# Performance work log

Hardware: AMD Instinct MI355X
Metric: run time of the kernel (lower is better)

## Reference

```python
import jax, jax.numpy as jnp
import numpy as np

B, C, H, W = 4, 256, 64, 64
DQK = C // 4


def setup_inputs() -> dict:
    key = jax.random.key(0)
    ks = jax.random.split(key, 5)
    s = 0.05
    x = jax.random.normal(ks[0], (B, C, H, W), dtype=jnp.float32)
    Wq = jax.random.normal(ks[1], (DQK, C), dtype=jnp.float32) * s
    Wk = jax.random.normal(ks[2], (DQK, C), dtype=jnp.float32) * s
    Wv = jax.random.normal(ks[3], (C, C), dtype=jnp.float32) * s
    bq = jnp.zeros((DQK,), jnp.float32)
    bk = jnp.zeros((DQK,), jnp.float32)
    bv = jnp.zeros((C,), jnp.float32)
    gamma = jnp.zeros((1,), jnp.float32)
    return {"x": x, "Wq": Wq, "bq": bq, "Wk": Wk, "bk": bk,
            "Wv": Wv, "bv": bv, "gamma": gamma}


def reference(x, Wq, bq, Wk, bk, Wv, bv, gamma):
    b, c, h, w = x.shape
    n = h * w
    xf = x.reshape(b, c, n)                      # [B, C, N]
    # 1x1 convs == per-pixel linear projections
    q = jnp.einsum('dc,bcn->bnd', Wq, xf) + bq   # [B, N, Dqk]
    k = jnp.einsum('dc,bcn->bdn', Wk, xf) + bk[None, :, None]  # [B, Dqk, N]
    v = jnp.einsum('ec,bcn->ben', Wv, xf) + bv[None, :, None]  # [B, C, N]
    energy = jnp.einsum('bnd,bdm->bnm', q, k)    # [B, N, N]
    attn = jax.nn.softmax(energy, axis=-1)       # softmax over keys
    # out[b,c,i] = sum_j v[b,c,j] * attn[b,i,j]
    out = jnp.einsum('bcj,bij->bci', v, attn)    # [B, C, N]
    out = out.reshape(b, c, h, w)
    return gamma * out + x
```

## Files before the change

kernel.cpp:

```cpp
#include <hip/hip_runtime.h>

#define B_ 4
#define C_ 256
#define N_ 4096
#define D_ 64

typedef __bf16 bf16x8 __attribute__((ext_vector_type(8)));
typedef float floatx4 __attribute__((ext_vector_type(4)));
typedef unsigned short ushort8v __attribute__((ext_vector_type(8)));
typedef unsigned short ushort4v __attribute__((ext_vector_type(4)));
typedef unsigned short ushort2v __attribute__((ext_vector_type(2)));

static __device__ __forceinline__ unsigned short f2bf(float f) {
    unsigned int u = __builtin_bit_cast(unsigned int, f);
    u += 0x7fffu + ((u >> 16) & 1u);
    return (unsigned short)(u >> 16);
}
static __device__ __forceinline__ float bf2f(unsigned short h) {
    unsigned int u = ((unsigned int)h) << 16;
    return __builtin_bit_cast(float, u);
}

#define GLOAD16(gp, lp)                                                      \
    __builtin_amdgcn_global_load_lds(                                        \
        (const __attribute__((address_space(1))) void*)(gp),                 \
        (__attribute__((address_space(3))) void*)(lp), 16, 0, 0)

__global__ __launch_bounds__(256) void convert_w(
    const float* __restrict__ Wq, const float* __restrict__ Wk,
    const float* __restrict__ Wv, unsigned short* __restrict__ WbfA)
{
    int tid = blockIdx.x * 256 + threadIdx.x;
    int p0  = tid * 4;
    int j0   = p0 & 7;
    int lane = (p0 >> 3) & 63;
    int sidx = p0 >> 9;
    int ft = sidx >> 3, ks = sidx & 7;
    int m  = lane & 15, g = lane >> 4;
    int f  = 16*ft + m;
    int c  = 32*ks + 8*g + j0;
    const float* src = (f < 64)  ? (Wq + (size_t)f * C_)
                     : (f < 128) ? (Wk + (size_t)(f - 64) * C_)
                                 : (Wv + (size_t)(f - 128) * C_);
    float4 v = *(const float4*)(src + c);
    ushort4v u;
    u[0] = f2bf(v.x); u[1] = f2bf(v.y); u[2] = f2bf(v.z); u[3] = f2bf(v.w);
    *(ushort4v*)(WbfA + p0) = u;
}

__global__ __launch_bounds__(256, 3) void proj_kernel(
    const float* __restrict__ x, const unsigned short* __restrict__ WbfA,
    const float* __restrict__ bq, const float* __restrict__ bk,
    const float* __restrict__ bv,
    unsigned short* __restrict__ Qg, unsigned short* __restrict__ Kg,
    unsigned short* __restrict__ Vg)
{
    __shared__ __align__(16) unsigned short smem[64 * 264];
    unsigned short* xs = smem;
    unsigned short* Lt = smem;

    const int n0 = blockIdx.x * 64;
    const int f0 = blockIdx.y * 128;
    const int b  = blockIdx.z;
    const int t  = threadIdx.x;
    const int w  = t >> 6;
    const int lane = t & 63;
    const int g  = lane >> 4;
    const int m  = lane & 15;

#pragma unroll
    for (int k = 0; k < 8; ++k) {
        int e  = t + 256 * k;
        int cp = e >> 4;
        int c  = 2 * cp;
        int n4 = (e & 15) * 4;
        float4 v0 = *(const float4*)(x + ((size_t)b*C_ + c    )*N_ + n0 + n4);
        float4 v1 = *(const float4*)(x + ((size_t)b*C_ + c + 1)*N_ + n0 + n4);
        float a0[4] = {v0.x, v0.y, v0.z, v0.w};
        float a1[4] = {v1.x, v1.y, v1.z, v1.w};
#pragma unroll
        for (int j = 0; j < 4; ++j) {
            int n = n4 + j;
            ushort2v u2;
            u2[0] = f2bf(a0[j]);
            u2[1] = f2bf(a1[j]);
            *(ushort2v*)&xs[n*264 + (((c >> 3) ^ (n & 7)) << 3) + (c & 7)] = u2;
        }
    }

    float bias_[2][4];
#pragma unroll
    for (int mt = 0; mt < 2; ++mt)
#pragma unroll
        for (int r = 0; r < 4; ++r) {
            int fg = f0 + 32*w + 16*mt + 4*g + r;
            bias_[mt][r] = (fg < 64) ? bq[fg]
                         : (fg < 128) ? bk[fg - 64] : bv[fg - 128];
        }

    const unsigned short* Wa0 = WbfA + (size_t)(((f0 >> 4) + 2*w    )*8)*512
                              + lane*8;
    const unsigned short* Wa1 = WbfA + (size_t)(((f0 >> 4) + 2*w + 1)*8)*512
                              + lane*8;

    floatx4 acc[2][4];
#pragma unroll
    for (int mt = 0; mt < 2; ++mt)
#pragma unroll
        for (int nt = 0; nt < 4; ++nt) acc[mt][nt] = (floatx4){0.f,0.f,0.f,0.f};

    __syncthreads();

#pragma unroll
    for (int ks = 0; ks < 8; ++ks) {
        bf16x8 af[2];
        af[0] = *(const bf16x8*)(Wa0 + ks*512);
        af[1] = *(const bf16x8*)(Wa1 + ks*512);
#pragma unroll
        for (int nt = 0; nt < 4; ++nt) {
            int n = 16*nt + m;
            bf16x8 bfr = *(const bf16x8*)
                &xs[n*264 + (((4*ks + g) ^ (n & 7)) << 3)];
#pragma unroll
            for (int mt = 0; mt < 2; ++mt)
                acc[mt][nt] = __builtin_amdgcn_mfma_f32_16x16x32_bf16(
                                  af[mt], bfr, acc[mt][nt], 0, 0, 0);
        }
    }

    __syncthreads();

#pragma unroll
    for (int mt = 0; mt < 2; ++mt)
#pragma unroll
        for (int nt = 0; nt < 4; ++nt)
#pragma unroll
            for (int r = 0; r < 4; ++r)
                Lt[(32*w + 16*mt + 4*g + r)*72 + 16*nt + m] =
                    f2bf(acc[mt][nt][r] + bias_[mt][r]);
    __syncthreads();

    if (f0 == 0) {
#pragma unroll
        for (int k = 0; k < 4; ++k) {
            int e   = t + 256 * k;
            int fq0 = (e >> 6) * 8;
            int nl  = e & 63;
            ushort8v u;
#pragma unroll
            for (int j = 0; j < 8; ++j) u[j] = Lt[(fq0 + j)*72 + nl];
            unsigned short* dst = (fq0 < 64)
                ? (Qg + ((size_t)b*N_ + n0 + nl)*D_ + fq0)
                : (Kg + ((size_t)b*N_ + n0 + nl)*D_ + (fq0 - 64));
            *(ushort8v*)dst = u;
        }
    } else {
        const int cb = f0 - 128;
#pragma unroll
        for (int k = 0; k < 4; ++k) {
            int e  = t + 256 * k;
            int fr = e >> 3;
            int n8 = (e & 7) * 8;
            ushort8v u = *(const ushort8v*)&Lt[fr*72 + n8];
            *(ushort8v*)(Vg + ((size_t)b*C_ + cb + fr)*N_ + n0 + n8) = u;
        }
    }
}

__global__ __launch_bounds__(256, 2) void flash_kernel(
    const unsigned short* __restrict__ Qg, const unsigned short* __restrict__ Kg,
    const unsigned short* __restrict__ Vg,
    unsigned short* __restrict__ Opart, float* __restrict__ ML)
{
    __shared__ __align__(16) unsigned short Vlds[32 * 512];
    __shared__ __align__(16) unsigned short Klds[2][8 * 512];
    __shared__ __align__(16) unsigned short PA[8 * 64 * 8];
    __shared__ float AL[64];

    const int g8   = blockIdx.x;
    const int tile = blockIdx.y;
    const int half = g8 & 1;
    const int b    = g8 >> 1;
    const int n0   = tile * 64;
    const int t    = threadIdx.x;
    const int w    = t >> 6;
    const int lane = t & 63;
    const int g    = lane >> 4;
    const int m    = lane & 15;

    const unsigned short* Qb = Qg + ((size_t)b*N_ + n0)*D_;
    const unsigned short* Kb = Kg + (size_t)b*N_*D_;
    const unsigned short* Vb = Vg + (size_t)b*C_*N_;

    const int cstart = half * 32;
    const int cend   = cstart + 32;

    bf16x8 qf[2];
#pragma unroll
    for (int ks = 0; ks < 2; ++ks)
        qf[ks] = *(const bf16x8*)(Qb + (size_t)(16*w + m)*D_ + 32*ks + 8*g);

    floatx4 accO[4][4];
#pragma unroll
    for (int rt = 0; rt < 4; ++rt)
#pragma unroll
        for (int ct = 0; ct < 4; ++ct)
            accO[rt][ct] = (floatx4){0.f, 0.f, 0.f, 0.f};

    float mrow = -1e30f, lrow = 0.f;

#pragma unroll
    for (int u = 0; u < 2; ++u) {
        const unsigned short* gp =
            Kb + (size_t)(cstart*64 + 16*w + m)*D_ + 32*u + 8*g;
        GLOAD16(gp, &Klds[0][(2*w + u) * 512]);
    }
    __syncthreads();

    for (int t64 = cstart; t64 < cend; ++t64) {
        const int j0 = t64 * 64;
        const int kb = (t64 - cstart) & 1;

#pragma unroll
        for (int u = 0; u < 8; ++u) {
            int sidx = 8*w + u;
            int ks   = sidx >> 4;
            int cb   = sidx & 15;
            const unsigned short* gp =
                Vb + (size_t)(16*cb + m)*N_ + j0 + 32*ks + 8*g;
            GLOAD16(gp, &Vlds[sidx * 512]);
        }
        if (t64 + 1 < cend) {
#pragma unroll
            for (int u = 0; u < 2; ++u) {
                const unsigned short* gp =
                    Kb + (size_t)((t64+1)*64 + 16*w + m)*D_ + 32*u + 8*g;
                GLOAD16(gp, &Klds[kb ^ 1][(2*w + u) * 512]);
            }
        }

        floatx4 accST[4];
#pragma unroll
        for (int jt = 0; jt < 4; ++jt) accST[jt] = (floatx4){0.f,0.f,0.f,0.f};
#pragma unroll
        for (int ks = 0; ks < 2; ++ks)
#pragma unroll
            for (int jt = 0; jt < 4; ++jt) {
                bf16x8 kfr = *(const bf16x8*)
                    &Klds[kb][(jt*2 + ks)*512 + lane*8];
                accST[jt] = __builtin_amdgcn_mfma_f32_16x16x32_bf16(
                                kfr, qf[ks], accST[jt], 0, 0, 0);
            }

        float mx = -1e30f;
#pragma unroll
        for (int jt = 0; jt < 4; ++jt)
#pragma unroll
            for (int r = 0; r < 4; ++r) mx = fmaxf(mx, accST[jt][r]);
        mx = fmaxf(mx, __shfl_xor(mx, 16));
        mx = fmaxf(mx, __shfl_xor(mx, 32));
        float mnew  = fmaxf(mrow, mx);
        float alpha = __expf(mrow - mnew);
        mrow = mnew;
        float p[4][4];
        float rs = 0.f;
#pragma unroll
        for (int jt = 0; jt < 4; ++jt)
#pragma unroll
            for (int r = 0; r < 4; ++r) {
                float e = __expf(accST[jt][r] - mnew);
                p[jt][r] = e;
                rs += e;
            }
        rs += __shfl_xor(rs, 16);
        rs += __shfl_xor(rs, 32);
        lrow = lrow * alpha + rs;

        if (g == 0) AL[16*w + m] = alpha;

#pragma unroll
        for (int jt = 0; jt < 4; ++jt) {
            ushort4v u;
#pragma unroll
            for (int r = 0; r < 4; ++r) u[r] = f2bf(p[jt][r]);
            int frag = (w*2 + (jt >> 1))*64 + 16*(2*(jt & 1) + (g >> 1)) + m;
            *(ushort4v*)&PA[frag*8 + 4*(g & 1)] = u;
        }

        __syncthreads();

#pragma unroll
        for (int rt = 0; rt < 4; ++rt) {
            floatx4 a4 = *(const floatx4*)&AL[16*rt + 4*g];
#pragma unroll
            for (int ct = 0; ct < 4; ++ct)
                accO[rt][ct] *= a4;
        }
#pragma unroll
        for (int ks = 0; ks < 2; ++ks) {
            bf16x8 pf[4];
#pragma unroll
            for (int rt = 0; rt < 4; ++rt)
                pf[rt] = *(const bf16x8*)&PA[((rt*2 + ks)*64 + lane)*8];
#pragma unroll
            for (int ct = 0; ct < 4; ++ct) {
                int sidx = ks*16 + 4*w + ct;
                bf16x8 vfrag = *(const bf16x8*)&Vlds[sidx*512 + lane*8];
#pragma unroll
                for (int rt = 0; rt < 4; ++rt)
                    accO[rt][ct] = __builtin_amdgcn_mfma_f32_16x16x32_bf16(
                                       pf[rt], vfrag, accO[rt][ct], 0, 0, 0);
            }
        }

        __syncthreads();
    }

    const size_t tbase = ((size_t)(half*B_ + b)*64 + tile);
    unsigned short* Ob = Opart + tbase * (C_ * 64);
    float* ml = ML + tbase * 128;

    if (g == 0) {
        ml[16*w + m]      = mrow;
        ml[64 + 16*w + m] = lrow;
    }

#pragma unroll
    for (int rt = 0; rt < 4; ++rt)
#pragma unroll
        for (int ct = 0; ct < 4; ++ct) {
            int c = 64*w + 16*ct + m;
            ushort4v u4;
#pragma unroll
            for (int r = 0; r < 4; ++r) u4[r] = f2bf(accO[rt][ct][r]);
            *(ushort4v*)(Ob + (size_t)c*64 + 16*rt + 4*g) = u4;
        }
}

__global__ __launch_bounds__(256) void combine_kernel(
    const unsigned short* __restrict__ Opart, const float* __restrict__ ML,
    const float* __restrict__ x, const float* __restrict__ gamma,
    float* __restrict__ out)
{
    __shared__ float sc0[64], sc1[64];
    const int tile  = blockIdx.x;
    const int chalf = blockIdx.y;
    const int b     = blockIdx.z;
    const int n0    = tile * 64;
    const int t     = threadIdx.x;

    if (t < 64) {
        const float* ml0 = ML + ((size_t)(0*B_ + b)*64 + tile)*128;
        const float* ml1 = ML + ((size_t)(1*B_ + b)*64 + tile)*128;
        float m0 = ml0[t], l0 = ml0[64 + t];
        float m1 = ml1[t], l1 = ml1[64 + t];
        float M  = fmaxf(m0, m1);
        float f0 = __expf(m0 - M), f1 = __expf(m1 - M);
        float L  = f0*l0 + f1*l1;
        float gm = gamma[0];
        sc0[t] = gm * f0 / L;
        sc1[t] = gm * f1 / L;
    }
    __syncthreads();

    const int nq = t & 15;
    const float* xb = x   + (size_t)b*C_*N_;
    float*       ob = out + (size_t)b*C_*N_;
    const unsigned short* O0 = Opart + ((size_t)(0*B_ + b)*64 + tile)*(C_*64);
    const unsigned short* O1 = Opart + ((size_t)(1*B_ + b)*64 + tile)*(C_*64);

    float s0[4], s1[4];
#pragma unroll
    for (int k = 0; k < 4; ++k) { s0[k] = sc0[4*nq + k]; s1[k] = sc1[4*nq + k]; }

#pragma unroll 4
    for (int i = 0; i < 8; ++i) {
        int c = 128*chalf + 16*i + (t >> 4);
        float4 x4 = *(const float4*)(xb + (size_t)c*N_ + n0 + 4*nq);
        ushort4v a4 = *(const ushort4v*)(O0 + (size_t)c*64 + 4*nq);
        ushort4v b4 = *(const ushort4v*)(O1 + (size_t)c*64 + 4*nq);
        float4 y;
        y.x = s0[0]*bf2f(a4[0]) + s1[0]*bf2f(b4[0]) + x4.x;
        y.y = s0[1]*bf2f(a4[1]) + s1[1]*bf2f(b4[1]) + x4.y;
        y.z = s0[2]*bf2f(a4[2]) + s1[2]*bf2f(b4[2]) + x4.z;
        y.w = s0[3]*bf2f(a4[3]) + s1[3]*bf2f(b4[3]) + x4.w;
        *(float4*)(ob + (size_t)c*N_ + n0 + 4*nq) = y;
    }
}

extern "C" void kernel_launch(void* const* d_in, const int* in_sizes, int n_in,
                              void* d_out, int out_size, void* d_ws, size_t ws_size,
                              hipStream_t stream) {
    const float* x     = (const float*)d_in[0];
    const float* Wq    = (const float*)d_in[1];
    const float* bq    = (const float*)d_in[2];
    const float* Wk    = (const float*)d_in[3];
    const float* bk    = (const float*)d_in[4];
    const float* Wv    = (const float*)d_in[5];
    const float* bv    = (const float*)d_in[6];
    const float* gamma = (const float*)d_in[7];
    float* out = (float*)d_out;

    unsigned short* Qg = (unsigned short*)d_ws;
    unsigned short* Kg = Qg + (size_t)B_*N_*D_;
    unsigned short* Vg = Kg + (size_t)B_*N_*D_;
    unsigned short* Op = Vg + (size_t)B_*C_*N_;
    float* ML = (float*)(Op + (size_t)2*B_*64*C_*64);
    unsigned short* WbfA = (unsigned short*)(ML + (size_t)2*B_*64*128);

    convert_w<<<dim3(96), 256, 0, stream>>>(Wq, Wk, Wv, WbfA);
    proj_kernel<<<dim3(64, 3, 4), 256, 0, stream>>>(x, WbfA, bq, bk, bv,
                                                    Qg, Kg, Vg);
    flash_kernel<<<dim3(8, 64), 256, 0, stream>>>(Qg, Kg, Vg, Op, ML);
    combine_kernel<<<dim3(64, 2, 4), 256, 0, stream>>>(Op, ML, x, gamma, out);
}
```

Measured before the change: 176.6 us.

## Double-buffer V in LDS and prefetch K tiles directly into registers

Restructures the flash-attention main loop so the V tile lives in two LDS buffers and the next tile's V is issued one iteration ahead. K is no longer staged through LDS; it is loaded straight into ping-pong register arrays. The loop is unrolled by two, with manual lgkmcnt waits and raw s_barrier replacing __syncthreads, and s_setprio raised around the PV MFMA block. This aims to hide global-load latency behind compute, at the cost of more LDS, more registers and reliance on implicit vmcnt ordering for correctness.

Measured after the change: 226.2 us. 1.28x slower.

```diff
diff --git a/kernel.cpp b/kernel.cpp
--- a/kernel.cpp
+++ b/kernel.cpp
@@ -172,8 +172,7 @@
     const unsigned short* __restrict__ Vg,
     unsigned short* __restrict__ Opart, float* __restrict__ ML)
 {
-    __shared__ __align__(16) unsigned short Vlds[32 * 512];
-    __shared__ __align__(16) unsigned short Klds[2][8 * 512];
+    __shared__ __align__(16) unsigned short Vlds[2][32 * 512];
     __shared__ __align__(16) unsigned short PA[8 * 64 * 8];
     __shared__ float AL[64];
 
@@ -193,7 +192,6 @@
     const unsigned short* Vb = Vg + (size_t)b*C_*N_;
 
     const int cstart = half * 32;
-    const int cend   = cstart + 32;
 
     bf16x8 qf[2];
 #pragma unroll
@@ -209,112 +207,123 @@
 
     float mrow = -1e30f, lrow = 0.f;
 
-#pragma unroll
-    for (int u = 0; u < 2; ++u) {
-        const unsigned short* gp =
-            Kb + (size_t)(cstart*64 + 16*w + m)*D_ + 32*u + 8*g;
-        GLOAD16(gp, &Klds[0][(2*w + u) * 512]);
-    }
-    __syncthreads();
-
-    for (int t64 = cstart; t64 < cend; ++t64) {
-        const int j0 = t64 * 64;
-        const int kb = (t64 - cstart) & 1;
-
-#pragma unroll
-        for (int u = 0; u < 8; ++u) {
-            int sidx = 8*w + u;
-            int ks   = sidx >> 4;
-            int cb   = sidx & 15;
-            const unsigned short* gp =
-                Vb + (size_t)(16*cb + m)*N_ + j0 + 32*ks + 8*g;
-            GLOAD16(gp, &Vlds[sidx * 512]);
-        }
-        if (t64 + 1 < cend) {
-#pragma unroll
-            for (int u = 0; u < 2; ++u) {
-                const unsigned short* gp =
-                    Kb + (size_t)((t64+1)*64 + 16*w + m)*D_ + 32*u + 8*g;
-                GLOAD16(gp, &Klds[kb ^ 1][(2*w + u) * 512]);
-            }
-        }
-
-        floatx4 accST[4];
-#pragma unroll
-        for (int jt = 0; jt < 4; ++jt) accST[jt] = (floatx4){0.f,0.f,0.f,0.f};
-#pragma unroll
-        for (int ks = 0; ks < 2; ++ks)
-#pragma unroll
-            for (int jt = 0; jt < 4; ++jt) {
-                bf16x8 kfr = *(const bf16x8*)
-                    &Klds[kb][(jt*2 + ks)*512 + lane*8];
-                accST[jt] = __builtin_amdgcn_mfma_f32_16x16x32_bf16(
-                                kfr, qf[ks], accST[jt], 0, 0, 0);
-            }
-
-        float mx = -1e30f;
-#pragma unroll
-        for (int jt = 0; jt < 4; ++jt)
-#pragma unroll
-            for (int r = 0; r < 4; ++r) mx = fmaxf(mx, accST[jt][r]);
-        mx = fmaxf(mx, __shfl_xor(mx, 16));
-        mx = fmaxf(mx, __shfl_xor(mx, 32));
-        float mnew  = fmaxf(mrow, mx);
-        float alpha = __expf(mrow - mnew);
-        mrow = mnew;
-        float p[4][4];
-        float rs = 0.f;
-#pragma unroll
-        for (int jt = 0; jt < 4; ++jt)
-#pragma unroll
-            for (int r = 0; r < 4; ++r) {
-                float e = __expf(accST[jt][r] - mnew);
-                p[jt][r] = e;
-                rs += e;
-            }
-        rs += __shfl_xor(rs, 16);
-        rs += __shfl_xor(rs, 32);
-        lrow = lrow * alpha + rs;
-
-        if (g == 0) AL[16*w + m] = alpha;
-
-#pragma unroll
-        for (int jt = 0; jt < 4; ++jt) {
-            ushort4v u;
-#pragma unroll
-            for (int r = 0; r < 4; ++r) u[r] = f2bf(p[jt][r]);
-            int frag = (w*2 + (jt >> 1))*64 + 16*(2*(jt & 1) + (g >> 1)) + m;
-            *(ushort4v*)&PA[frag*8 + 4*(g & 1)] = u;
-        }
-
-        __syncthreads();
-
-#pragma unroll
-        for (int rt = 0; rt < 4; ++rt) {
-            floatx4 a4 = *(const floatx4*)&AL[16*rt + 4*g];
-#pragma unroll
-            for (int ct = 0; ct < 4; ++ct)
-                accO[rt][ct] *= a4;
-        }
-#pragma unroll
-        for (int ks = 0; ks < 2; ++ks) {
-            bf16x8 pf[4];
-#pragma unroll
-            for (int rt = 0; rt < 4; ++rt)
-                pf[rt] = *(const bf16x8*)&PA[((rt*2 + ks)*64 + lane)*8];
-#pragma unroll
-            for (int ct = 0; ct < 4; ++ct) {
-                int sidx = ks*16 + 4*w + ct;
-                bf16x8 vfrag = *(const bf16x8*)&Vlds[sidx*512 + lane*8];
-#pragma unroll
-                for (int rt = 0; rt < 4; ++rt)
-                    accO[rt][ct] = __builtin_amdgcn_mfma_f32_16x16x32_bf16(
-                                       pf[rt], vfrag, accO[rt][ct], 0, 0, 0);
-            }
-        }
-
-        __syncthreads();
-    }
+    bf16x8 krA[8], krB[8];
+    int tn = cstart;
+
+#define ISSUE_V(TT, VBW) do {                                                \
+    const size_t j0v = (size_t)(TT) * 64;                                    \
+    _Pragma("unroll")                                                        \
+    for (int u_ = 0; u_ < 8; ++u_) {                                         \
+        int sdx = 8*w + u_;                                                  \
+        int ksv = sdx >> 4;                                                  \
+        int cbv = sdx & 15;                                                  \
+        const unsigned short* gp =                                           \
+            Vb + (size_t)(16*cbv + m)*N_ + j0v + 32*ksv + 8*g;               \
+        GLOAD16(gp, &Vlds[VBW][sdx * 512]);                                  \
+    } } while (0)
+
+#define LOAD_K(TT, KR) do {                                                  \
+    _Pragma("unroll")                                                        \
+    for (int sdx = 0; sdx < 8; ++sdx)                                        \
+        KR[sdx] = *(const bf16x8*)(Kb                                        \
+            + (size_t)((TT)*64 + 16*(sdx >> 1) + m)*D_                       \
+            + 32*(sdx & 1) + 8*g);                                           \
+    } while (0)
+
+    ISSUE_V(tn, 0);
+    LOAD_K(tn, krA);
+    ++tn;
+
+#define FBODY(KU, KN, VB_, PRE_) do {                                        \
+    if (PRE_) { ISSUE_V(tn, (VB_) ^ 1); LOAD_K(tn, KN); ++tn; }              \
+      \
+    floatx4 accST[4];                                                        \
+    _Pragma("unroll")                                                        \
+    for (int jt = 0; jt < 4; ++jt) accST[jt] = (floatx4){0.f,0.f,0.f,0.f};   \
+    _Pragma("unroll")                                                        \
+    for (int ks = 0; ks < 2; ++ks)                                           \
+        _Pragma("unroll")                                                    \
+        for (int jt = 0; jt < 4; ++jt)                                       \
+            accST[jt] = __builtin_amdgcn_mfma_f32_16x16x32_bf16(             \
+                            KU[jt*2 + ks], qf[ks], accST[jt], 0, 0, 0);      \
+                \
+    float mx = -1e30f;                                                       \
+    _Pragma("unroll")                                                        \
+    for (int jt = 0; jt < 4; ++jt)                                           \
+        _Pragma("unroll")                                                    \
+        for (int r = 0; r < 4; ++r) mx = fmaxf(mx, accST[jt][r]);            \
+    mx = fmaxf(mx, __shfl_xor(mx, 16));                                      \
+    mx = fmaxf(mx, __shfl_xor(mx, 32));                                      \
+    float mnew  = fmaxf(mrow, mx);                                           \
+    float alpha = __expf(mrow - mnew);                                       \
+    mrow = mnew;                                                             \
+    float p_[4][4];                                                          \
+    float rs = 0.f;                                                          \
+    _Pragma("unroll")                                                        \
+    for (int jt = 0; jt < 4; ++jt)                                           \
+        _Pragma("unroll")                                                    \
+        for (int r = 0; r < 4; ++r) {                                        \
+            float e_ = __expf(accST[jt][r] - mnew);                          \
+            p_[jt][r] = e_;                                                  \
+            rs += e_;                                                        \
+        }                                                                    \
+    rs += __shfl_xor(rs, 16);                                                \
+    rs += __shfl_xor(rs, 32);                                                \
+    lrow = lrow * alpha + rs;                                                \
+    if (g == 0) AL[16*w + m] = alpha;                                        \
+                         \
+    _Pragma("unroll")                                                        \
+    for (int jt = 0; jt < 4; ++jt) {                                         \
+        ushort4v u4_;                                                        \
+        _Pragma("unroll")                                                    \
+        for (int r = 0; r < 4; ++r) u4_[r] = f2bf(p_[jt][r]);                \
+        int frag = (w*2 + (jt >> 1))*64 + 16*(2*(jt & 1) + (g >> 1)) + m;    \
+        *(ushort4v*)&PA[frag*8 + 4*(g & 1)] = u4_;                           \
+    }                                                                        \
+                \
+    asm volatile("s_waitcnt lgkmcnt(0)" ::: "memory");                       \
+    __builtin_amdgcn_s_barrier();                                            \
+                                                              \
+    _Pragma("unroll")                                                        \
+    for (int rt = 0; rt < 4; ++rt) {                                         \
+        floatx4 a4 = *(const floatx4*)&AL[16*rt + 4*g];                      \
+        _Pragma("unroll")                                                    \
+        for (int ct = 0; ct < 4; ++ct) accO[rt][ct] *= a4;                   \
+    }                                                                        \
+                                                           \
+    __builtin_amdgcn_s_setprio(1);                                           \
+    _Pragma("unroll")                                                        \
+    for (int ks = 0; ks < 2; ++ks) {                                         \
+        bf16x8 pf[4];                                                        \
+        _Pragma("unroll")                                                    \
+        for (int rt = 0; rt < 4; ++rt)                                       \
+            pf[rt] = *(const bf16x8*)&PA[((rt*2 + ks)*64 + lane)*8];         \
+        _Pragma("unroll")                                                    \
+        for (int ct = 0; ct < 4; ++ct) {                                     \
+            int sdx = ks*16 + 4*w + ct;                                      \
+            bf16x8 vfrag = *(const bf16x8*)&Vlds[VB_][sdx*512 + lane*8];     \
+            _Pragma("unroll")                                                \
+            for (int rt = 0; rt < 4; ++rt)                                   \
+                accO[rt][ct] = __builtin_amdgcn_mfma_f32_16x16x32_bf16(      \
+                                   pf[rt], vfrag, accO[rt][ct], 0, 0, 0);    \
+        }                                                                    \
+    }                                                                        \
+    __builtin_amdgcn_s_setprio(0);                                           \
+             \
+    asm volatile("s_waitcnt lgkmcnt(0)" ::: "memory");                       \
+    __builtin_amdgcn_s_barrier();                                            \
+} while (0)
+
+    for (int trip = 0; trip < 15; ++trip) {
+        FBODY(krA, krB, 0, 1);
+        FBODY(krB, krA, 1, 1);
+    }
+    FBODY(krA, krB, 0, 1);
+    FBODY(krB, krA, 1, 0);
+
+#undef FBODY
+#undef LOAD_K
+#undef ISSUE_V
 
     const size_t tbase = ((size_t)(half*B_ + b)*64 + tile);
     unsigned short* Ob = Opart + tbase * (C_ * 64);
```

## Double flash query tile to 128 rows with 512-thread blocks sharing K/V LDS

Applied to the files above, without the earlier changes.

The flash kernel now processes 128 queries per block with 8 waves instead of 64 queries with 4 waves. Each K/V tile loaded into LDS is reused by twice as many query rows, which halves global-to-LDS traffic per query. Waves split into two query groups and four channel groups for the PV product. The partial-output layout and the combine kernel are resized to match. Grid size halves, so there are fewer, larger blocks, which may reduce latency hiding or balance across CUs.

After: 179.4 us. No clear change (+1.6%).

```diff
diff --git a/kernel.cpp b/kernel.cpp
--- a/kernel.cpp
+++ b/kernel.cpp
@@ -167,26 +167,28 @@
     }
 }
 
-__global__ __launch_bounds__(256, 2) void flash_kernel(
+__global__ __launch_bounds__(512, 2) void flash_kernel(
     const unsigned short* __restrict__ Qg, const unsigned short* __restrict__ Kg,
     const unsigned short* __restrict__ Vg,
     unsigned short* __restrict__ Opart, float* __restrict__ ML)
 {
     __shared__ __align__(16) unsigned short Vlds[32 * 512];
     __shared__ __align__(16) unsigned short Klds[2][8 * 512];
-    __shared__ __align__(16) unsigned short PA[8 * 64 * 8];
-    __shared__ float AL[64];
+    __shared__ __align__(16) unsigned short PA[16 * 64 * 8];
+    __shared__ float AL[128];
 
     const int g8   = blockIdx.x;
     const int tile = blockIdx.y;
     const int half = g8 & 1;
     const int b    = g8 >> 1;
-    const int n0   = tile * 64;
+    const int n0   = tile * 128;
     const int t    = threadIdx.x;
     const int w    = t >> 6;
     const int lane = t & 63;
     const int g    = lane >> 4;
     const int m    = lane & 15;
+    const int wq   = w >> 2;
+    const int cq   = w & 3;
 
     const unsigned short* Qb = Qg + ((size_t)b*N_ + n0)*D_;
     const unsigned short* Kb = Kg + (size_t)b*N_*D_;
@@ -209,11 +211,10 @@
 
     float mrow = -1e30f, lrow = 0.f;
 
-#pragma unroll
-    for (int u = 0; u < 2; ++u) {
+    {
         const unsigned short* gp =
-            Kb + (size_t)(cstart*64 + 16*w + m)*D_ + 32*u + 8*g;
-        GLOAD16(gp, &Klds[0][(2*w + u) * 512]);
+            Kb + (size_t)(cstart*64 + 16*(w >> 1) + m)*D_ + 32*(w & 1) + 8*g;
+        GLOAD16(gp, &Klds[0][w * 512]);
     }
     __syncthreads();
 
@@ -222,8 +223,8 @@
         const int kb = (t64 - cstart) & 1;
 
 #pragma unroll
-        for (int u = 0; u < 8; ++u) {
-            int sidx = 8*w + u;
+        for (int u = 0; u < 4; ++u) {
+            int sidx = 4*w + u;
             int ks   = sidx >> 4;
             int cb   = sidx & 15;
             const unsigned short* gp =
@@ -231,12 +232,10 @@
             GLOAD16(gp, &Vlds[sidx * 512]);
         }
         if (t64 + 1 < cend) {
-#pragma unroll
-            for (int u = 0; u < 2; ++u) {
-                const unsigned short* gp =
-                    Kb + (size_t)((t64+1)*64 + 16*w + m)*D_ + 32*u + 8*g;
-                GLOAD16(gp, &Klds[kb ^ 1][(2*w + u) * 512]);
-            }
+            const unsigned short* gp =
+                Kb + (size_t)((t64+1)*64 + 16*(w >> 1) + m)*D_
+                   + 32*(w & 1) + 8*g;
+            GLOAD16(gp, &Klds[kb ^ 1][w * 512]);
         }
 
         floatx4 accST[4];
@@ -291,7 +290,7 @@
 
 #pragma unroll
         for (int rt = 0; rt < 4; ++rt) {
-            floatx4 a4 = *(const floatx4*)&AL[16*rt + 4*g];
+            floatx4 a4 = *(const floatx4*)&AL[64*wq + 16*rt + 4*g];
 #pragma unroll
             for (int ct = 0; ct < 4; ++ct)
                 accO[rt][ct] *= a4;
@@ -301,10 +300,11 @@
             bf16x8 pf[4];
 #pragma unroll
             for (int rt = 0; rt < 4; ++rt)
-                pf[rt] = *(const bf16x8*)&PA[((rt*2 + ks)*64 + lane)*8];
+                pf[rt] = *(const bf16x8*)
+                    &PA[((8*wq + rt*2 + ks)*64 + lane)*8];
 #pragma unroll
             for (int ct = 0; ct < 4; ++ct) {
-                int sidx = ks*16 + 4*w + ct;
+                int sidx = ks*16 + 4*cq + ct;
                 bf16x8 vfrag = *(const bf16x8*)&Vlds[sidx*512 + lane*8];
 #pragma unroll
                 for (int rt = 0; rt < 4; ++rt)
@@ -316,24 +316,25 @@
         __syncthreads();
     }
 
-    const size_t tbase = ((size_t)(half*B_ + b)*64 + tile);
-    unsigned short* Ob = Opart + tbase * (C_ * 64);
-    float* ml = ML + tbase * 128;
+    const size_t tbase = ((size_t)(half*B_ + b)*32 + tile);
+    unsigned short* Ob = Opart + tbase * (C_ * 128);
+    float* ml = ML + tbase * 256;
 
     if (g == 0) {
-        ml[16*w + m]      = mrow;
-        ml[64 + 16*w + m] = lrow;
+        ml[16*w + m]       = mrow;
+        ml[128 + 16*w + m] = lrow;
     }
 
 #pragma unroll
     for (int rt = 0; rt < 4; ++rt)
 #pragma unroll
         for (int ct = 0; ct < 4; ++ct) {
-            int c = 64*w + 16*ct + m;
+            int c  = 64*cq + 16*ct + m;
+            int q0 = 64*wq + 16*rt + 4*g;
             ushort4v u4;
 #pragma unroll
             for (int r = 0; r < 4; ++r) u4[r] = f2bf(accO[rt][ct][r]);
-            *(ushort4v*)(Ob + (size_t)c*64 + 16*rt + 4*g) = u4;
+            *(ushort4v*)(Ob + (size_t)c*128 + q0) = u4;
         }
 }
 
@@ -342,18 +343,18 @@
     const float* __restrict__ x, const float* __restrict__ gamma,
     float* __restrict__ out)
 {
-    __shared__ float sc0[64], sc1[64];
+    __shared__ float sc0[128], sc1[128];
     const int tile  = blockIdx.x;
     const int chalf = blockIdx.y;
     const int b     = blockIdx.z;
-    const int n0    = tile * 64;
+    const int n0    = tile * 128;
     const int t     = threadIdx.x;
 
-    if (t < 64) {
-        const float* ml0 = ML + ((size_t)(0*B_ + b)*64 + tile)*128;
-        const float* ml1 = ML + ((size_t)(1*B_ + b)*64 + tile)*128;
-        float m0 = ml0[t], l0 = ml0[64 + t];
-        float m1 = ml1[t], l1 = ml1[64 + t];
+    if (t < 128) {
+        const float* ml0 = ML + ((size_t)(0*B_ + b)*32 + tile)*256;
+        const float* ml1 = ML + ((size_t)(1*B_ + b)*32 + tile)*256;
+        float m0 = ml0[t], l0 = ml0[128 + t];
+        float m1 = ml1[t], l1 = ml1[128 + t];
         float M  = fmaxf(m0, m1);
         float f0 = __expf(m0 - M), f1 = __expf(m1 - M);
         float L  = f0*l0 + f1*l1;
@@ -363,22 +364,23 @@
     }
     __syncthreads();
 
-    const int nq = t & 15;
+    const int nq = t & 31;
+    const int cl = t >> 5;
     const float* xb = x   + (size_t)b*C_*N_;
     float*       ob = out + (size_t)b*C_*N_;
-    const unsigned short* O0 = Opart + ((size_t)(0*B_ + b)*64 + tile)*(C_*64);
-    const unsigned short* O1 = Opart + ((size_t)(1*B_ + b)*64 + tile)*(C_*64);
+    const unsigned short* O0 = Opart + ((size_t)(0*B_ + b)*32 + tile)*(C_*128);
+    const unsigned short* O1 = Opart + ((size_t)(1*B_ + b)*32 + tile)*(C_*128);
 
     float s0[4], s1[4];
 #pragma unroll
     for (int k = 0; k < 4; ++k) { s0[k] = sc0[4*nq + k]; s1[k] = sc1[4*nq + k]; }
 
 #pragma unroll 4
-    for (int i = 0; i < 8; ++i) {
-        int c = 128*chalf + 16*i + (t >> 4);
+    for (int i = 0; i < 16; ++i) {
+        int c = 128*chalf + 8*i + cl;
         float4 x4 = *(const float4*)(xb + (size_t)c*N_ + n0 + 4*nq);
-        ushort4v a4 = *(const ushort4v*)(O0 + (size_t)c*64 + 4*nq);
-        ushort4v b4 = *(const ushort4v*)(O1 + (size_t)c*64 + 4*nq);
+        ushort4v a4 = *(const ushort4v*)(O0 + (size_t)c*128 + 4*nq);
+        ushort4v b4 = *(const ushort4v*)(O1 + (size_t)c*128 + 4*nq);
         float4 y;
         y.x = s0[0]*bf2f(a4[0]) + s1[0]*bf2f(b4[0]) + x4.x;
         y.y = s0[1]*bf2f(a4[1]) + s1[1]*bf2f(b4[1]) + x4.y;
@@ -405,12 +407,12 @@
     unsigned short* Kg = Qg + (size_t)B_*N_*D_;
     unsigned short* Vg = Kg + (size_t)B_*N_*D_;
     unsigned short* Op = Vg + (size_t)B_*C_*N_;
-    float* ML = (float*)(Op + (size_t)2*B_*64*C_*64);
-    unsigned short* WbfA = (unsigned short*)(ML + (size_t)2*B_*64*128);
+    float* ML = (float*)(Op + (size_t)2*B_*32*C_*128);
+    unsigned short* WbfA = (unsigned short*)(ML + (size_t)2*B_*32*256);
 
     convert_w<<<dim3(96), 256, 0, stream>>>(Wq, Wk, Wv, WbfA);
     proj_kernel<<<dim3(64, 3, 4), 256, 0, stream>>>(x, WbfA, bq, bk, bv,
                                                     Qg, Kg, Vg);
-    flash_kernel<<<dim3(8, 64), 256, 0, stream>>>(Qg, Kg, Vg, Op, ML);
-    combine_kernel<<<dim3(64, 2, 4), 256, 0, stream>>>(Op, ML, x, gamma, out);
-}
+    flash_kernel<<<dim3(8, 32), 512, 0, stream>>>(Qg, Kg, Vg, Op, ML);
+    combine_kernel<<<dim3(32, 2, 4), 256, 0, stream>>>(Op, ML, x, gamma, out);
+}
```
